# Kernel optimization log

Measured on AMD Instinct MI355X. Metric: run time of the kernel, lower is better.

## Reference

```python
import jax, jax.numpy as jnp
import numpy as np

D = 768          # hidden_size
N_HEADS = 12
HEAD_DIM = D // N_HEADS  # 64
WINDOW = 128 // 2        # local_attention // 2 = 64 tokens each side
ROPE_THETA = 10000.0     # local_rope_theta


def _rope_freqs(T, dtype=jnp.float32):
    # complex rotation factors e^{i * pos * inv_freq}, shape [T, HEAD_DIM//2]
    inv_freq = 1.0 / (ROPE_THETA ** (jnp.arange(0, HEAD_DIM, 2, dtype=dtype) / HEAD_DIM))
    ang = jnp.arange(T, dtype=dtype)[:, None] * inv_freq[None, :]
    return jnp.exp(1j * ang.astype(jnp.complex64))


def _apply_rope(x, freqs):
    # x: [B, T, N, H]; split into (2, H//2) pairs as in the source reshape
    B, T, N, H = x.shape
    pairs = x.reshape(B, T, N, 2, H // 2)
    c = pairs[..., 0, :] + 1j * pairs[..., 1, :]          # [B,T,N,H//2]
    rot = c * freqs[None, :, None, :]                      # broadcast over B, heads
    out = jnp.stack([jnp.real(rot), jnp.imag(rot)], axis=-1)  # [B,T,N,H//2,2]
    return out.reshape(B, T, N, H)  # attention_scaling = 1.0 for default rope


def setup_inputs() -> dict:
    key = jax.random.key(0)
    k1, k2, k3 = jax.random.split(key, 3)
    B, T = 4, 2048
    hidden_states = jax.random.normal(k1, (B, T, D), dtype=jnp.float32)
    attention_mask = jnp.ones((B, T), dtype=jnp.int32)
    Wqkv = jax.random.normal(k2, (3 * D, D), dtype=jnp.float32) * (1.0 / np.sqrt(D))
    Wo = jax.random.normal(k3, (D, D), dtype=jnp.float32) * (1.0 / np.sqrt(D))
    return {"hidden_states": hidden_states, "attention_mask": attention_mask,
            "Wqkv": Wqkv, "Wo": Wo}


def reference(hidden_states, attention_mask, Wqkv, Wo):
    B, T, _ = hidden_states.shape
    # fused QKV projection (no bias in ModernBERT)
    qkv = jnp.einsum('btd,ed->bte', hidden_states, Wqkv)   # [B,T,3D]
    q, k, v = jnp.split(qkv, 3, axis=-1)
    to_heads = lambda x: x.reshape(B, T, N_HEADS, HEAD_DIM)
    q, k, v = to_heads(q), to_heads(k), to_heads(v)
    # rotary embedding (complex multiply)
    freqs = _rope_freqs(T)
    q = _apply_rope(q, freqs)
    k = _apply_rope(k, freqs)
    # sliding-window + padding mask
    pos = jnp.arange(T)
    window = jnp.abs(pos[:, None] - pos[None, :]) <= WINDOW   # [T,T]
    pad = attention_mask.astype(jnp.bool_)                    # [B,T]
    allowed = window[None, None, :, :] & pad[:, None, :, None] & pad[:, None, None, :]
    # eager SDPA
    scale = 1.0 / np.sqrt(HEAD_DIM)
    scores = jnp.einsum('bqnh,bknh->bnqk', q, k) * scale      # [B,N,T,T]
    scores = jnp.where(allowed, scores, jnp.finfo(scores.dtype).min)
    probs = jax.nn.softmax(scores, axis=-1)
    attn = jnp.einsum('bnqk,bknh->bqnh', probs, v)            # [B,T,N,H]
    attn = attn.reshape(B, T, D)
    return jnp.einsum('btd,ed->bte', attn, Wo)                # output proj
```

## Files before the change

kernel.cpp:

```cpp
#include <hip/hip_runtime.h>
#include <hip/hip_bf16.h>
#include <math.h>

#define BATCH 4
#define SEQ   2048
#define DMODEL 768
#define NHEADS 12
#define HDIM  64
#define WIN   64
#define QKV_LD 2304

typedef __attribute__((ext_vector_type(8))) short bf16x8;
typedef __attribute__((ext_vector_type(4))) float f32x4;

typedef __attribute__((address_space(1))) const unsigned int guint;
typedef __attribute__((address_space(3))) unsigned int luint;

__device__ inline void gl_lds16(const __hip_bfloat16* g, __hip_bfloat16* l) {
    __builtin_amdgcn_global_load_lds((guint*)g, (luint*)l, 16, 0, 0);
}

__device__ inline void to_out(float* p, float v) { *p = v; }
__device__ inline void to_out(__hip_bfloat16* p, float v) { *p = __float2bfloat16(v); }

#define N4_HID  (BATCH * SEQ * DMODEL / 4)
#define N4_WQKV (QKV_LD * DMODEL / 4)
#define N4_WO   (DMODEL * DMODEL / 4)
#define N_ROPE  (SEQ * 32)
#define SETUP_TOTAL (N4_HID + N4_WQKV + N4_WO + N_ROPE)

__device__ inline void cast4(const float* in, __hip_bfloat16* out, int i) {
    float4 v = ((const float4*)in)[i];
    union { ushort4 u; __hip_bfloat16 h[4]; } o;
    o.h[0] = __float2bfloat16(v.x); o.h[1] = __float2bfloat16(v.y);
    o.h[2] = __float2bfloat16(v.z); o.h[3] = __float2bfloat16(v.w);
    ((ushort4*)out)[i] = o.u;
}

__global__ __launch_bounds__(256) void setup_kernel(const float* __restrict__ hidden,
                                                    const float* __restrict__ Wqkv,
                                                    const float* __restrict__ Wo,
                                                    __hip_bfloat16* __restrict__ hid_bf,
                                                    __hip_bfloat16* __restrict__ wqkv_bf,
                                                    __hip_bfloat16* __restrict__ wo_bf,
                                                    float2* __restrict__ tab) {
    int id = blockIdx.x * 256 + threadIdx.x;
    if (id < N4_HID) {
        cast4(hidden, hid_bf, id);
    } else if (id < N4_HID + N4_WQKV) {
        cast4(Wqkv, wqkv_bf, id - N4_HID);
    } else if (id < N4_HID + N4_WQKV + N4_WO) {
        cast4(Wo, wo_bf, id - N4_HID - N4_WQKV);
    } else if (id < SETUP_TOTAL) {
        int idx = id - (N4_HID + N4_WQKV + N4_WO);
        int t = idx >> 5, j = idx & 31;
        const float L2T_OVER_32 = 13.287712379549449f / 32.0f;
        float inv = exp2f(-(float)j * L2T_OVER_32);
        float s, c;
        sincosf((float)t * inv, &s, &c);
        tab[idx] = make_float2(c, s);
    }
}

template <typename OutT, int NWN>
__global__ __launch_bounds__(256) void gemm_nt_bf16(const __hip_bfloat16* __restrict__ A,
                                                    const __hip_bfloat16* __restrict__ B,
                                                    OutT* __restrict__ C,
                                                    int lda, int ldb, int ldc, int K,
                                                    const float2* __restrict__ rope_tab) {
    constexpr int BN  = 64 * NWN;
    constexpr int NWM = 4 / NWN;
    constexpr int WM  = 128 / NWM;
    constexpr int MI  = WM / 16;

    __shared__ __align__(16) __hip_bfloat16 As[128 * 64];
    __shared__ __align__(16) __hip_bfloat16 Bs[BN * 64];

    const int tid  = threadIdx.x;
    const int lane = tid & 63;
    const int wave = tid >> 6;
    const int wm   = wave / NWN;
    const int wn   = wave % NWN;
    const int fr   = lane & 15;
    const int quad = lane >> 4;

    const int bid = blockIdx.x;
    const int x   = bid & 7;
    const int j   = bid >> 3;
    const int m0  = (x * 8 + (j & 7)) * 128;
    const int n0  = (j >> 3) * BN;

    f32x4 acc[MI][4];
#pragma unroll
    for (int i = 0; i < MI; i++)
#pragma unroll
        for (int jj = 0; jj < 4; jj++) acc[i][jj] = (f32x4){0.f, 0.f, 0.f, 0.f};

    for (int k0 = 0; k0 < K; k0 += 64) {
        __syncthreads();
#pragma unroll
        for (int c = 0; c < 4; c++) {
            int t = (wave * 4 + c) * 64 + lane;
            int row = t >> 3, ch = t & 7;
            int gcol = (ch ^ (row & 7)) * 8;
            gl_lds16(A + (size_t)(m0 + row) * lda + k0 + gcol, As + t * 8);
        }
#pragma unroll
        for (int c = 0; c < 2 * NWN; c++) {
            int t = (wave * 2 * NWN + c) * 64 + lane;
            int row = t >> 3, ch = t & 7;
            int gcol = (ch ^ (row & 7)) * 8;
            gl_lds16(B + (size_t)(n0 + row) * ldb + k0 + gcol, Bs + t * 8);
        }
        __syncthreads();

#pragma unroll
        for (int ks = 0; ks < 2; ks++) {
            bf16x8 af[MI], bf_[4];
#pragma unroll
            for (int mi = 0; mi < MI; mi++) {
                int row = wm * WM + mi * 16 + fr;
                int pos = (ks * 4 + quad) ^ (row & 7);
                af[mi] = *(const bf16x8*)(As + row * 64 + pos * 8);
            }
#pragma unroll
            for (int ni = 0; ni < 4; ni++) {
                int row = wn * 64 + ni * 16 + fr;
                int pos = (ks * 4 + quad) ^ (row & 7);
                bf_[ni] = *(const bf16x8*)(Bs + row * 64 + pos * 8);
            }
#pragma unroll
            for (int mi = 0; mi < MI; mi++)
#pragma unroll
                for (int ni = 0; ni < 4; ni++)
                    acc[mi][ni] = __builtin_amdgcn_mfma_f32_16x16x32_bf16(af[mi], bf_[ni], acc[mi][ni], 0, 0, 0);
        }
    }

    const int b0 = n0 + wn * 64;
    if (rope_tab != nullptr && b0 < 2 * DMODEL) {
#pragma unroll
        for (int mi = 0; mi < MI; mi++) {
#pragma unroll
            for (int r = 0; r < 4; r++) {
                int t = (m0 + wm * WM + mi * 16 + quad * 4 + r) & (SEQ - 1);
#pragma unroll
                for (int ni = 0; ni < 2; ni++) {
                    float2 cs = rope_tab[t * 32 + ni * 16 + fr];
                    float x0 = acc[mi][ni][r], x1 = acc[mi][ni + 2][r];
                    acc[mi][ni][r]     = x0 * cs.x - x1 * cs.y;
                    acc[mi][ni + 2][r] = x0 * cs.y + x1 * cs.x;
                }
            }
        }
    }

#pragma unroll
    for (int mi = 0; mi < MI; mi++)
#pragma unroll
        for (int ni = 0; ni < 4; ni++) {
            f32x4 v = acc[mi][ni];
            int gc = b0 + ni * 16 + fr;
            size_t rbase = (size_t)(m0 + wm * WM + mi * 16 + quad * 4);
#pragma unroll
            for (int r = 0; r < 4; r++)
                to_out(&C[(rbase + r) * ldc + gc], v[r]);
        }
}

#define PLD  192

__global__ __launch_bounds__(256) void attn_kernel(const __hip_bfloat16* __restrict__ qkv,
                                                   const int* __restrict__ mask,
                                                   __hip_bfloat16* __restrict__ attn) {
    __shared__ __align__(16) char smem[49152];
    __hip_bfloat16* Ks = (__hip_bfloat16*)smem;
    __hip_bfloat16* Pb = (__hip_bfloat16*)smem;
    __hip_bfloat16* Vt = (__hip_bfloat16*)(smem + 24576);

    const int tid  = threadIdx.x;
    const int lane = tid & 63;
    const int wave = tid >> 6;
    const int fr   = lane & 15;
    const int quad = lane >> 4;

    const int bid  = blockIdx.x;
    const int x    = bid & 7;
    const int j    = bid >> 3;
    const int b    = x >> 1;
    const int q0   = ((x & 1) * 16 + (j & 15)) * 64;
    const int head = j >> 4;

    const int klo = max(0, q0 - WIN);
    const int khi = min(SEQ, q0 + 64 + WIN);
    const int nk  = khi - klo;
    const int nt  = nk >> 4;
    const int nkc = nk >> 5;

    const size_t rowbase = (size_t)(b * SEQ) * QKV_LD + head * HDIM;

    for (int task = tid; task < nk * 8; task += 256) {
        int row = task >> 3, g = task & 7;
        uint4 v = *(const uint4*)(qkv + rowbase + (size_t)(klo + row) * QKV_LD + DMODEL + g * 8);
        *(uint4*)(Ks + row * 64 + (g ^ (row & 7)) * 8) = v;
    }
    {
        int h = lane;
        const __hip_bfloat16* vb = qkv + rowbase + 2 * DMODEL + h;
        int ng = nk >> 3;
        for (int g = wave; g < ng; g += 4) {
            unsigned int u0, u1, u2, u3;
            {
                unsigned short a0 = *(const unsigned short*)(vb + (size_t)(klo + g * 8 + 0) * QKV_LD);
                unsigned short a1 = *(const unsigned short*)(vb + (size_t)(klo + g * 8 + 1) * QKV_LD);
                unsigned short a2 = *(const unsigned short*)(vb + (size_t)(klo + g * 8 + 2) * QKV_LD);
                unsigned short a3 = *(const unsigned short*)(vb + (size_t)(klo + g * 8 + 3) * QKV_LD);
                unsigned short a4 = *(const unsigned short*)(vb + (size_t)(klo + g * 8 + 4) * QKV_LD);
                unsigned short a5 = *(const unsigned short*)(vb + (size_t)(klo + g * 8 + 5) * QKV_LD);
                unsigned short a6 = *(const unsigned short*)(vb + (size_t)(klo + g * 8 + 6) * QKV_LD);
                unsigned short a7 = *(const unsigned short*)(vb + (size_t)(klo + g * 8 + 7) * QKV_LD);
                u0 = (unsigned int)a0 | ((unsigned int)a1 << 16);
                u1 = (unsigned int)a2 | ((unsigned int)a3 << 16);
                u2 = (unsigned int)a4 | ((unsigned int)a5 << 16);
                u3 = (unsigned int)a6 | ((unsigned int)a7 << 16);
            }
            int cs = g ^ (h & 7);
            *(uint4*)(Vt + h * PLD + cs * 8) = make_uint4(u0, u1, u2, u3);
        }
    }

    const int qrow0 = q0 + wave * 16;
    bf16x8 aq0 = *(const bf16x8*)(qkv + rowbase + (size_t)(qrow0 + fr) * QKV_LD + quad * 8);
    bf16x8 aq1 = *(const bf16x8*)(qkv + rowbase + (size_t)(qrow0 + fr) * QKV_LD + 32 + quad * 8);

    const int* mb = mask + b * SEQ;
    int mq[4];
#pragma unroll
    for (int r = 0; r < 4; r++) mq[r] = mb[qrow0 + quad * 4 + r];

    __syncthreads();

    f32x4 sc[12];
#pragma unroll
    for (int kt = 0; kt < 12; kt++) sc[kt] = (f32x4){-1e30f, -1e30f, -1e30f, -1e30f};

#pragma unroll
    for (int kt = 0; kt < 12; kt++) {
        if (kt < nt) {
            int krow = kt * 16 + fr;
            int kg = klo + krow;
            int p0 = (quad) ^ (krow & 7);
            int p1 = (4 + quad) ^ (krow & 7);
            bf16x8 bk0 = *(const bf16x8*)(Ks + krow * 64 + p0 * 8);
            bf16x8 bk1 = *(const bf16x8*)(Ks + krow * 64 + p1 * 8);
            f32x4 a = (f32x4){0.f, 0.f, 0.f, 0.f};
            a = __builtin_amdgcn_mfma_f32_16x16x32_bf16(aq0, bk0, a, 0, 0, 0);
            a = __builtin_amdgcn_mfma_f32_16x16x32_bf16(aq1, bk1, a, 0, 0, 0);
            int mk = mb[kg];
            f32x4 s;
#pragma unroll
            for (int r = 0; r < 4; r++) {
                int qg = qrow0 + quad * 4 + r;
                bool ok = (abs(qg - kg) <= WIN) && (mk != 0) && (mq[r] != 0);
                s[r] = ok ? a[r] * 0.125f : -1e30f;
            }
            sc[kt] = s;
        }
    }

    f32x4 mx = sc[0];
#pragma unroll
    for (int kt = 1; kt < 12; kt++)
#pragma unroll
        for (int r = 0; r < 4; r++) mx[r] = fmaxf(mx[r], sc[kt][r]);
#pragma unroll
    for (int off = 8; off >= 1; off >>= 1)
#pragma unroll
        for (int r = 0; r < 4; r++) mx[r] = fmaxf(mx[r], __shfl_xor(mx[r], off));

    f32x4 sum = (f32x4){0.f, 0.f, 0.f, 0.f};
#pragma unroll
    for (int kt = 0; kt < 12; kt++)
#pragma unroll
        for (int r = 0; r < 4; r++) {
            float e = __expf(sc[kt][r] - mx[r]);
            sc[kt][r] = e;
            sum[r] += e;
        }
#pragma unroll
    for (int off = 8; off >= 1; off >>= 1)
#pragma unroll
        for (int r = 0; r < 4; r++) sum[r] += __shfl_xor(sum[r], off);
    f32x4 rs;
#pragma unroll
    for (int r = 0; r < 4; r++) rs[r] = 1.0f / sum[r];

    __syncthreads();
#pragma unroll
    for (int kt = 0; kt < 12; kt++) {
        if (kt < nt) {
#pragma unroll
            for (int r = 0; r < 4; r++) {
                int prow = wave * 16 + quad * 4 + r;
                int c = kt * 2 + (fr >> 3);
                int cs = c ^ (prow & 7);
                Pb[prow * PLD + cs * 8 + (fr & 7)] = __float2bfloat16(sc[kt][r] * rs[r]);
            }
        }
    }
    __syncthreads();

    f32x4 o[4];
#pragma unroll
    for (int ht = 0; ht < 4; ht++) o[ht] = (f32x4){0.f, 0.f, 0.f, 0.f};

#pragma unroll
    for (int kc = 0; kc < 6; kc++) {
        if (kc < nkc) {
            int cs = (kc * 4 + quad) ^ (fr & 7);
            bf16x8 ap = *(const bf16x8*)(Pb + (wave * 16 + fr) * PLD + cs * 8);
#pragma unroll
            for (int ht = 0; ht < 4; ht++) {
                bf16x8 bv = *(const bf16x8*)(Vt + (ht * 16 + fr) * PLD + cs * 8);
                o[ht] = __builtin_amdgcn_mfma_f32_16x16x32_bf16(ap, bv, o[ht], 0, 0, 0);
            }
        }
    }

    __hip_bfloat16* ob = attn + (size_t)(b * SEQ + qrow0) * DMODEL + head * HDIM;
#pragma unroll
    for (int r = 0; r < 4; r++)
#pragma unroll
        for (int ht = 0; ht < 4; ht++)
            ob[(size_t)(quad * 4 + r) * DMODEL + ht * 16 + fr] = __float2bfloat16(o[ht][r]);
}

extern "C" void kernel_launch(void* const* d_in, const int* in_sizes, int n_in,
                              void* d_out, int out_size, void* d_ws, size_t ws_size,
                              hipStream_t stream) {
    const float* hidden = (const float*)d_in[0];
    const int*   mask   = (const int*)d_in[1];
    const float* Wqkv   = (const float*)d_in[2];
    const float* Wo     = (const float*)d_in[3];
    float* out = (float*)d_out;

    char* w = (char*)d_ws;
    __hip_bfloat16* qkv_bf  = (__hip_bfloat16*)(w);
    __hip_bfloat16* hid_bf  = (__hip_bfloat16*)(w + 37748736);
    __hip_bfloat16* wqkv_bf = (__hip_bfloat16*)(w + 50331648);
    __hip_bfloat16* wo_bf   = (__hip_bfloat16*)(w + 53870592);
    __hip_bfloat16* attn_bf = (__hip_bfloat16*)(w + 55050240);
    float2*         tab     = (float2*)(w + 67633152);

    setup_kernel<<<SETUP_TOTAL / 256, 256, 0, stream>>>(hidden, Wqkv, Wo,
                                                        hid_bf, wqkv_bf, wo_bf, tab);

    gemm_nt_bf16<__hip_bfloat16, 2><<<18 * 64, 256, 0, stream>>>(hid_bf, wqkv_bf, qkv_bf,
                                                                 DMODEL, DMODEL, QKV_LD, DMODEL, tab);

    attn_kernel<<<(SEQ / 64) * NHEADS * BATCH, 256, 0, stream>>>(qkv_bf, mask, attn_bf);

    gemm_nt_bf16<float, 1><<<12 * 64, 256, 0, stream>>>(attn_bf, wo_bf, out,
                                                        DMODEL, DMODEL, DMODEL, DMODEL, nullptr);
}
```

Before: 182.3 us.

## Double-buffer GEMM LDS tiles with K-step 32 and async prefetch

Splits the GEMM's LDS staging into two buffers, each holding a K=32 slice. The next slice is prefetched with global_load_lds while MFMAs run on the current one, and each iteration now needs only a single barrier instead of two. The aim is to hide global-load latency behind compute; the smaller tiles also cut the LDS footprint. In exchange, barriers become twice as frequent per unit of K, each iteration does less MFMA work, and the narrower 4-chunk XOR swizzle may cause more LDS bank conflicts.

```diff
diff --git a/kernel.cpp b/kernel.cpp
--- a/kernel.cpp
+++ b/kernel.cpp
@@ -73,8 +73,8 @@
     constexpr int WM  = 128 / NWM;
     constexpr int MI  = WM / 16;
 
-    __shared__ __align__(16) __hip_bfloat16 As[128 * 64];
-    __shared__ __align__(16) __hip_bfloat16 Bs[BN * 64];
+    __shared__ __align__(16) __hip_bfloat16 As[2][128 * 32];
+    __shared__ __align__(16) __hip_bfloat16 Bs[2][BN * 32];
 
     const int tid  = threadIdx.x;
     const int lane = tid & 63;
@@ -96,45 +96,48 @@
 #pragma unroll
         for (int jj = 0; jj < 4; jj++) acc[i][jj] = (f32x4){0.f, 0.f, 0.f, 0.f};
 
-    for (int k0 = 0; k0 < K; k0 += 64) {
+    auto stage = [&](int buf, int k0) {
+#pragma unroll
+        for (int c = 0; c < 2; c++) {
+            int t = (wave * 2 + c) * 64 + lane;
+            int row = t >> 2, ch = t & 3;
+            int gcol = (ch ^ (row & 3)) * 8;
+            gl_lds16(A + (size_t)(m0 + row) * lda + k0 + gcol, &As[buf][t * 8]);
+        }
+#pragma unroll
+        for (int c = 0; c < NWN; c++) {
+            int t = (wave * NWN + c) * 64 + lane;
+            int row = t >> 2, ch = t & 3;
+            int gcol = (ch ^ (row & 3)) * 8;
+            gl_lds16(B + (size_t)(n0 + row) * ldb + k0 + gcol, &Bs[buf][t * 8]);
+        }
+    };
+
+    const int NIT = K >> 5;
+    stage(0, 0);
+    for (int i = 0; i < NIT; i++) {
+        const int cur = i & 1;
         __syncthreads();
-#pragma unroll
-        for (int c = 0; c < 4; c++) {
-            int t = (wave * 4 + c) * 64 + lane;
-            int row = t >> 3, ch = t & 7;
-            int gcol = (ch ^ (row & 7)) * 8;
-            gl_lds16(A + (size_t)(m0 + row) * lda + k0 + gcol, As + t * 8);
-        }
-#pragma unroll
-        for (int c = 0; c < 2 * NWN; c++) {
-            int t = (wave * 2 * NWN + c) * 64 + lane;
-            int row = t >> 3, ch = t & 7;
-            int gcol = (ch ^ (row & 7)) * 8;
-            gl_lds16(B + (size_t)(n0 + row) * ldb + k0 + gcol, Bs + t * 8);
-        }
-        __syncthreads();
-
-#pragma unroll
-        for (int ks = 0; ks < 2; ks++) {
-            bf16x8 af[MI], bf_[4];
-#pragma unroll
-            for (int mi = 0; mi < MI; mi++) {
-                int row = wm * WM + mi * 16 + fr;
-                int pos = (ks * 4 + quad) ^ (row & 7);
-                af[mi] = *(const bf16x8*)(As + row * 64 + pos * 8);
-            }
-#pragma unroll
-            for (int ni = 0; ni < 4; ni++) {
-                int row = wn * 64 + ni * 16 + fr;
-                int pos = (ks * 4 + quad) ^ (row & 7);
-                bf_[ni] = *(const bf16x8*)(Bs + row * 64 + pos * 8);
-            }
-#pragma unroll
-            for (int mi = 0; mi < MI; mi++)
-#pragma unroll
-                for (int ni = 0; ni < 4; ni++)
-                    acc[mi][ni] = __builtin_amdgcn_mfma_f32_16x16x32_bf16(af[mi], bf_[ni], acc[mi][ni], 0, 0, 0);
-        }
+        if (i + 1 < NIT) stage(1 - cur, (i + 1) * 32);
+
+        bf16x8 af[MI], bf_[4];
+#pragma unroll
+        for (int mi = 0; mi < MI; mi++) {
+            int row = wm * WM + mi * 16 + fr;
+            int pos = quad ^ (row & 3);
+            af[mi] = *(const bf16x8*)&As[cur][row * 32 + pos * 8];
+        }
+#pragma unroll
+        for (int ni = 0; ni < 4; ni++) {
+            int row = wn * 64 + ni * 16 + fr;
+            int pos = quad ^ (row & 3);
+            bf_[ni] = *(const bf16x8*)&Bs[cur][row * 32 + pos * 8];
+        }
+#pragma unroll
+        for (int mi = 0; mi < MI; mi++)
+#pragma unroll
+            for (int ni = 0; ni < 4; ni++)
+                acc[mi][ni] = __builtin_amdgcn_mfma_f32_16x16x32_bf16(af[mi], bf_[ni], acc[mi][ni], 0, 0, 0);
     }
 
     const int b0 = n0 + wn * 64;
```

Result: slower. 186.9 us (+2.5%).

## Pre-transpose V into a separate buffer to vectorize attention V loads

Applied to the files above, without the earlier changes.

Adds a kernel that transposes each head's V block through shared memory into a [B,H,HDIM,SEQ] buffer. The attention kernel then loads V with 16-byte vector loads instead of eight scalar 2-byte strided gathers per lane. This also removes the threefold redundant strided V reads across overlapping windows, at the cost of an extra launch and an extra round trip of V through memory.

```diff
diff --git a/kernel.cpp b/kernel.cpp
--- a/kernel.cpp
+++ b/kernel.cpp
@@ -168,9 +168,49 @@
         }
 }
 
+__global__ __launch_bounds__(256) void vtrans_kernel(const __hip_bfloat16* __restrict__ qkv,
+                                                     __hip_bfloat16* __restrict__ vT) {
+    __shared__ __hip_bfloat16 Vs[64][72];
+
+    const int bid  = blockIdx.x;
+    const int x    = bid & 7;
+    const int j    = bid >> 3;
+    const int b    = x >> 1;
+    const int t0   = ((x & 1) * 16 + (j & 15)) * 64;
+    const int head = j >> 4;
+    const int tid  = threadIdx.x;
+
+#pragma unroll
+    for (int it = 0; it < 2; it++) {
+        int task = tid + it * 256;
+        int row = task >> 3, c8 = (task & 7) * 8;
+        uint4 v = *(const uint4*)(qkv + (size_t)(b * SEQ + t0 + row) * QKV_LD
+                                  + 2 * DMODEL + head * HDIM + c8);
+        *(uint4*)(&Vs[row][c8]) = v;
+    }
+    __syncthreads();
+
+#pragma unroll
+    for (int it = 0; it < 2; it++) {
+        int task = tid + it * 256;
+        int h = task >> 3, t8 = (task & 7) * 8;
+        unsigned short e[8];
+#pragma unroll
+        for (int jj = 0; jj < 8; jj++)
+            e[jj] = *(const unsigned short*)&Vs[t8 + jj][h];
+        uint4 o;
+        o.x = (unsigned int)e[0] | ((unsigned int)e[1] << 16);
+        o.y = (unsigned int)e[2] | ((unsigned int)e[3] << 16);
+        o.z = (unsigned int)e[4] | ((unsigned int)e[5] << 16);
+        o.w = (unsigned int)e[6] | ((unsigned int)e[7] << 16);
+        *(uint4*)(vT + ((size_t)(b * NHEADS + head) * HDIM + h) * SEQ + t0 + t8) = o;
+    }
+}
+
 #define PLD  192
 
 __global__ __launch_bounds__(256) void attn_kernel(const __hip_bfloat16* __restrict__ qkv,
+                                                   const __hip_bfloat16* __restrict__ vT,
                                                    const int* __restrict__ mask,
                                                    __hip_bfloat16* __restrict__ attn) {
     __shared__ __align__(16) char smem[49152];
@@ -205,27 +245,19 @@
         *(uint4*)(Ks + row * 64 + (g ^ (row & 7)) * 8) = v;
     }
     {
-        int h = lane;
-        const __hip_bfloat16* vb = qkv + rowbase + 2 * DMODEL + h;
-        int ng = nk >> 3;
-        for (int g = wave; g < ng; g += 4) {
-            unsigned int u0, u1, u2, u3;
-            {
-                unsigned short a0 = *(const unsigned short*)(vb + (size_t)(klo + g * 8 + 0) * QKV_LD);
-                unsigned short a1 = *(const unsigned short*)(vb + (size_t)(klo + g * 8 + 1) * QKV_LD);
-                unsigned short a2 = *(const unsigned short*)(vb + (size_t)(klo + g * 8 + 2) * QKV_LD);
-                unsigned short a3 = *(const unsigned short*)(vb + (size_t)(klo + g * 8 + 3) * QKV_LD);
-                unsigned short a4 = *(const unsigned short*)(vb + (size_t)(klo + g * 8 + 4) * QKV_LD);
-                unsigned short a5 = *(const unsigned short*)(vb + (size_t)(klo + g * 8 + 5) * QKV_LD);
-                unsigned short a6 = *(const unsigned short*)(vb + (size_t)(klo + g * 8 + 6) * QKV_LD);
-                unsigned short a7 = *(const unsigned short*)(vb + (size_t)(klo + g * 8 + 7) * QKV_LD);
-                u0 = (unsigned int)a0 | ((unsigned int)a1 << 16);
-                u1 = (unsigned int)a2 | ((unsigned int)a3 << 16);
-                u2 = (unsigned int)a4 | ((unsigned int)a5 << 16);
-                u3 = (unsigned int)a6 | ((unsigned int)a7 << 16);
-            }
-            int cs = g ^ (h & 7);
-            *(uint4*)(Vt + h * PLD + cs * 8) = make_uint4(u0, u1, u2, u3);
+        const __hip_bfloat16* vTb = vT + (size_t)(b * NHEADS + head) * HDIM * SEQ + klo;
+        if (nk == 192) {
+            for (int task = tid; task < 64 * 24; task += 256) {
+                int h = task / 24, g = task % 24;
+                uint4 v = *(const uint4*)(vTb + (size_t)h * SEQ + g * 8);
+                *(uint4*)(Vt + h * PLD + (g ^ (h & 7)) * 8) = v;
+            }
+        } else {
+            for (int task = tid; task < 64 * 16; task += 256) {
+                int h = task >> 4, g = task & 15;
+                uint4 v = *(const uint4*)(vTb + (size_t)h * SEQ + g * 8);
+                *(uint4*)(Vt + h * PLD + (g ^ (h & 7)) * 8) = v;
+            }
         }
     }
 
@@ -351,6 +383,7 @@
     __hip_bfloat16* wo_bf   = (__hip_bfloat16*)(w + 53870592);
     __hip_bfloat16* attn_bf = (__hip_bfloat16*)(w + 55050240);
     float2*         tab     = (float2*)(w + 67633152);
+    __hip_bfloat16* vT      = (__hip_bfloat16*)(w + 68157440);
 
     setup_kernel<<<SETUP_TOTAL / 256, 256, 0, stream>>>(hidden, Wqkv, Wo,
                                                         hid_bf, wqkv_bf, wo_bf, tab);
@@ -358,7 +391,9 @@
     gemm_nt_bf16<__hip_bfloat16, 2><<<18 * 64, 256, 0, stream>>>(hid_bf, wqkv_bf, qkv_bf,
                                                                  DMODEL, DMODEL, QKV_LD, DMODEL, tab);
 
-    attn_kernel<<<(SEQ / 64) * NHEADS * BATCH, 256, 0, stream>>>(qkv_bf, mask, attn_bf);
+    vtrans_kernel<<<1536, 256, 0, stream>>>(qkv_bf, vT);
+
+    attn_kernel<<<(SEQ / 64) * NHEADS * BATCH, 256, 0, stream>>>(qkv_bf, vT, mask, attn_bf);
 
     gemm_nt_bf16<float, 1><<<12 * 64, 256, 0, stream>>>(attn_bf, wo_bf, out,
                                                         DMODEL, DMODEL, DMODEL, DMODEL, nullptr);
```

Measured after the change: 188.7 us. 1.03x slower.
